# Kernel optimization log

Measured on AMD Instinct MI355X. Metric: run time of the kernel, lower is better.

Reference implementation:

```python
import jax, jax.numpy as jnp
import numpy as np

D_MODEL = 1024
N_HEADS = 16
HEAD_DIM = D_MODEL // N_HEADS


def setup_inputs() -> dict:
    key = jax.random.key(0)
    ks = jax.random.split(key, 5)
    B, T = 4, 4096
    x = jax.random.normal(ks[0], (B, T, D_MODEL), dtype=jnp.float32)
    s = 1.0 / np.sqrt(D_MODEL)
    Wqkv = jax.random.normal(ks[1], (D_MODEL, 3 * D_MODEL), dtype=jnp.float32) * s
    bqkv = jnp.zeros((3 * D_MODEL,), dtype=jnp.float32)
    Wout = jax.random.normal(ks[2], (D_MODEL, D_MODEL), dtype=jnp.float32) * s
    bout = jnp.zeros((D_MODEL,), dtype=jnp.float32)
    return {"x": x, "Wqkv": Wqkv, "bqkv": bqkv, "Wout": Wout, "bout": bout}


def _feature_map(x):
    # elu(x) + 1  (strictly positive feature map)
    return jax.nn.elu(x) + 1.0


def reference(x, Wqkv, bqkv, Wout, bout):
    B, T, C = x.shape
    H, D = N_HEADS, HEAD_DIM
    qkv = x @ Wqkv + bqkv                      # [B,T,3C]
    qkv = qkv.reshape(B, T, 3, H, D)
    qkv = jnp.transpose(qkv, (2, 0, 3, 1, 4))  # [3,B,H,T,D]
    q, k, v = qkv[0], qkv[1], qkv[2]
    scale = D ** 0.25
    q_m = _feature_map(q / scale)
    k_m = _feature_map(k / scale)
    kv = jnp.einsum('bhtd,bhtm->bhdm', k_m, v)     # [B,H,D,D]
    out = jnp.einsum('bhtd,bhdm->bhtm', q_m, kv)   # [B,H,T,D]
    z = q_m.sum(axis=-1, keepdims=True)            # note: sum over feature dim (as in source)
    out = out / (z + 1e-6)
    out = jnp.transpose(out, (0, 2, 1, 3)).reshape(B, T, C)
    return out @ Wout + bout
```

## Files before the change

### kernel.cpp

```cpp
#include <hip/hip_runtime.h>
#include <hip/hip_bf16.h>
#include <math.h>

#define B_ 4
#define T_ 4096
#define H_ 16
#define D_ 64
#define C_ 1024
#define BT_ (B_*T_)

using short8  = __attribute__((ext_vector_type(8))) short;
using floatx4 = __attribute__((ext_vector_type(4))) float;

__device__ __forceinline__ float feature_map(float x) {
    return x > 0.0f ? x + 1.0f : __expf(x);
}
__device__ __forceinline__ unsigned short f2bf(float x) {
    union { __hip_bfloat16 b; unsigned short u; } c;
    c.b = __float2bfloat16(x);
    return c.u;
}
__device__ __forceinline__ void async16(const void* g, void* l) {
    __builtin_amdgcn_global_load_lds(
        (const __attribute__((address_space(1))) void*)g,
        (__attribute__((address_space(3))) void*)l, 16, 0, 0);
}
__device__ __forceinline__ const char* sel3(const char* a0, const char* a1,
                                            const char* a2, int t) {
    return t == 0 ? a0 : (t == 1 ? a1 : a2);
}

__global__ __launch_bounds__(256)
void convert_x_kernel(const float4* __restrict__ x, ushort* __restrict__ xb)
{
    const size_t n = (size_t)BT_ * C_ / 8;
    for (size_t i = (size_t)blockIdx.x * 256 + threadIdx.x; i < n;
         i += (size_t)2048 * 256) {
        const float4 a = x[2 * i], b = x[2 * i + 1];
        short8 r;
        r[0] = (short)f2bf(a.x); r[1] = (short)f2bf(a.y);
        r[2] = (short)f2bf(a.z); r[3] = (short)f2bf(a.w);
        r[4] = (short)f2bf(b.x); r[5] = (short)f2bf(b.y);
        r[6] = (short)f2bf(b.z); r[7] = (short)f2bf(b.w);
        *reinterpret_cast<short8*>(&xb[i * 8]) = r;
    }
}

__global__ __launch_bounds__(256)
void transpose_w_kernel(const float* __restrict__ Wqkv, ushort* __restrict__ WqkvT,
                        const float* __restrict__ Wout, ushort* __restrict__ WoutT)
{
    __shared__ float t[32][33];
    const bool qkv = blockIdx.x < 96;
    const float* W  = qkv ? Wqkv : Wout;
    ushort* WT      = qkv ? WqkvT : WoutT;
    const int N     = qkv ? 3 * C_ : C_;
    const int n0 = (qkv ? blockIdx.x : blockIdx.x - 96) * 32, k0 = blockIdx.y * 32;
    const int r = threadIdx.x >> 5, c = threadIdx.x & 31;
    #pragma unroll
    for (int i = 0; i < 4; i++)
        t[r + 8 * i][c] = W[(size_t)(k0 + r + 8 * i) * N + n0 + c];
    __syncthreads();
    #pragma unroll
    for (int i = 0; i < 4; i++)
        WT[(size_t)(n0 + r + 8 * i) * C_ + k0 + c] = f2bf(t[c][r + 8 * i]);
}

#define BAR()    __builtin_amdgcn_s_barrier()
#define WAITDS() do { asm volatile("s_waitcnt lgkmcnt(0)" ::: "memory"); \
                      __builtin_amdgcn_sched_barrier(0); } while(0)
#define VM6()    do { asm volatile("s_waitcnt vmcnt(6)" ::: "memory"); \
                      __builtin_amdgcn_sched_barrier(0); } while(0)

#define LDA(slot, mf, ks, buf) \
    aR[slot][ks] = *(const short8*)(smem + (buf)*32768 + ((mf)>>2)*16384 + \
                                    aRowB + ((mf)&3)*2048 + cks##ks)
#define LDB(nf, ks, buf) \
    bR[nf][ks] = *(const short8*)(smem + 65536 + (buf)*32768 + ((nf)>>1)*16384 + \
                                  bRowB + ((nf)&1)*2048 + cks##ks)
#define LDA8(MB, BUF) do { \
    LDA(0, MB+0, 0, BUF); LDA(0, MB+0, 1, BUF); \
    LDA(1, MB+1, 0, BUF); LDA(1, MB+1, 1, BUF); \
    LDA(2, MB+2, 0, BUF); LDA(2, MB+2, 1, BUF); \
    LDA(3, MB+3, 0, BUF); LDA(3, MB+3, 1, BUF); } while(0)
#define LDB4(NF, BUF) do { \
    LDB(NF+0, 0, BUF); LDB(NF+0, 1, BUF); \
    LDB(NF+1, 0, BUF); LDB(NF+1, 1, BUF); } while(0)

#define MM(mf, nf, ks, slot) \
    acc[mf][nf] = __builtin_amdgcn_mfma_f32_16x16x32_bf16( \
        aR[slot][ks], bR[nf][ks], acc[mf][nf], 0, 0, 0)
#define MFMAQ(MB, NF) do { \
    MM(MB+0,NF+0,0,0); MM(MB+1,NF+0,0,1); MM(MB+2,NF+0,0,2); MM(MB+3,NF+0,0,3); \
    MM(MB+0,NF+1,0,0); MM(MB+1,NF+1,0,1); MM(MB+2,NF+1,0,2); MM(MB+3,NF+1,0,3); \
    MM(MB+0,NF+0,1,0); MM(MB+1,NF+0,1,1); MM(MB+2,NF+0,1,2); MM(MB+3,NF+0,1,3); \
    MM(MB+0,NF+1,1,0); MM(MB+1,NF+1,1,1); MM(MB+2,NF+1,1,2); MM(MB+3,NF+1,1,3); \
} while(0)

#define STGA(h, G, buf) do { int _g = (G); if (_g >= NTILE*16) _g -= NTILE*16; \
    const char* _b = sel3(Ab0, Ab1, Ab2, _g >> 4); const int _w = (_g & 15) * 128; \
    async16(_b + aOf##h##0 + _w, smem + (buf)*32768 + (h)*16384 + wv*1024); \
    async16(_b + aOf##h##1 + _w, smem + (buf)*32768 + (h)*16384 + 8192 + wv*1024); \
} while(0)
#define STGB(h, G, buf) do { int _g = (G); if (_g >= NTILE*16) _g -= NTILE*16; \
    const char* _b = sel3(Bb0, Bb1, Bb2, _g >> 4); const int _w = (_g & 15) * 128; \
    async16(_b + bOf##h##0 + _w, smem + 65536 + (buf)*32768 + (h)*16384 + wv*1024); \
    async16(_b + bOf##h##1 + _w, smem + 65536 + (buf)*32768 + (h)*16384 + 8192 + wv*1024); \
} while(0)

#define ITERBODY(GB) \
    const int g1 = (GB) + 2*it + 1, g2 = (GB) + 2*it + 2, g3 = (GB) + 2*it + 3; \
     BAR(); LDA8(0, 0); LDB4(0, 0); STGA(1, g1, 1); \
    WAITDS(); __builtin_amdgcn_s_setprio(1); MFMAQ(0, 0); \
    __builtin_amdgcn_s_setprio(0); \
     BAR(); LDB4(2, 0); STGA(0, g2, 0); \
    WAITDS(); __builtin_amdgcn_s_setprio(1); MFMAQ(0, 2); \
    __builtin_amdgcn_s_setprio(0); \
     BAR(); LDA8(4, 0); STGB(0, g2, 0); \
    WAITDS(); __builtin_amdgcn_s_setprio(1); MFMAQ(4, 2); \
    __builtin_amdgcn_s_setprio(0); \
     BAR(); STGB(1, g2, 0); \
    WAITDS(); __builtin_amdgcn_s_setprio(1); MFMAQ(4, 0); \
    __builtin_amdgcn_s_setprio(0); VM6(); \
     BAR(); LDA8(0, 1); LDB4(0, 1); STGA(1, g2, 0); \
    WAITDS(); __builtin_amdgcn_s_setprio(1); MFMAQ(0, 0); \
    __builtin_amdgcn_s_setprio(0); \
     BAR(); LDB4(2, 1); STGA(0, g3, 1); \
    WAITDS(); __builtin_amdgcn_s_setprio(1); MFMAQ(0, 2); \
    __builtin_amdgcn_s_setprio(0); \
     BAR(); LDA8(4, 1); STGB(0, g3, 1); \
    WAITDS(); __builtin_amdgcn_s_setprio(1); MFMAQ(4, 2); \
    __builtin_amdgcn_s_setprio(0); \
     BAR(); STGB(1, g3, 1); \
    WAITDS(); __builtin_amdgcn_s_setprio(1); MFMAQ(4, 0); \
    __builtin_amdgcn_s_setprio(0); VM6();

template<int EPI>
__device__ __forceinline__ void gemm_epilogue(
    floatx4 (&acc)[8][4], const float (&bv)[4],
    int mBase, int nBase, int wm, int wn, int lr, int quad,
    ushort* __restrict__ q_out, ushort* __restrict__ kT_out,
    ushort* __restrict__ vT_out, float* __restrict__ f_out)
{
    if (EPI == 0) {
        const float inv_scale = 0.35355339059327373f;
        const int seg = nBase >> 10;
        if (seg == 0) {
            #pragma unroll
            for (int mf = 0; mf < 8; mf++)
                #pragma unroll
                for (int i = 0; i < 4; i++) {
                    float f0 = feature_map((acc[mf][0][i] + bv[0]) * inv_scale);
                    float f1 = feature_map((acc[mf][1][i] + bv[1]) * inv_scale);
                    float f2 = feature_map((acc[mf][2][i] + bv[2]) * inv_scale);
                    float f3 = feature_map((acc[mf][3][i] + bv[3]) * inv_scale);
                    float z = f0 + f1 + f2 + f3;
                    z += __shfl_xor(z, 1); z += __shfl_xor(z, 2);
                    z += __shfl_xor(z, 4); z += __shfl_xor(z, 8);
                    const float inv = 1.0f / (z + 1e-6f);
                    const int t = mBase + wm * 128 + mf * 16 + quad * 4 + i;
                    const int cbase = nBase + wn * 64 + lr;
                    q_out[(size_t)t * C_ + cbase]      = f2bf(f0 * inv);
                    q_out[(size_t)t * C_ + cbase + 16] = f2bf(f1 * inv);
                    q_out[(size_t)t * C_ + cbase + 32] = f2bf(f2 * inv);
                    q_out[(size_t)t * C_ + cbase + 48] = f2bf(f3 * inv);
                }
        } else {
            ushort* dstT = (seg == 1) ? kT_out : vT_out;
            #pragma unroll
            for (int nf = 0; nf < 4; nf++) {
                const int c = (nBase + wn * 64 + nf * 16 + lr) & 1023;
                #pragma unroll
                for (int mf = 0; mf < 8; mf++) {
                    float v0 = acc[mf][nf][0] + bv[nf], v1 = acc[mf][nf][1] + bv[nf];
                    float v2 = acc[mf][nf][2] + bv[nf], v3 = acc[mf][nf][3] + bv[nf];
                    if (seg == 1) {
                        v0 = feature_map(v0 * inv_scale); v1 = feature_map(v1 * inv_scale);
                        v2 = feature_map(v2 * inv_scale); v3 = feature_map(v3 * inv_scale);
                    }
                    const int tt = mBase + wm * 128 + mf * 16 + quad * 4;
                    *(ushort4*)&dstT[(size_t)c * BT_ + tt] =
                        make_ushort4(f2bf(v0), f2bf(v1), f2bf(v2), f2bf(v3));
                }
            }
        }
    } else {
        #pragma unroll
        for (int nf = 0; nf < 4; nf++) {
            const int c = nBase + wn * 64 + nf * 16 + lr;
            #pragma unroll
            for (int mf = 0; mf < 8; mf++)
                #pragma unroll
                for (int i = 0; i < 4; i++) {
                    const int row = mBase + wm * 128 + mf * 16 + quad * 4 + i;
                    f_out[(size_t)row * C_ + c] = acc[mf][nf][i] + bv[nf];
                }
        }
    }
    #pragma unroll
    for (int i = 0; i < 8; i++)
        #pragma unroll
        for (int j = 0; j < 4; j++) acc[i][j] = (floatx4)0.0f;
}

template<int EPI, int NBX, int NTILE>
__device__ __forceinline__ void gemm_body(
    const ushort* __restrict__ A, const ushort* __restrict__ Bm,
    const float* __restrict__ bias,
    ushort* __restrict__ q_out, ushort* __restrict__ kT_out,
    ushort* __restrict__ vT_out, float* __restrict__ f_out)
{
    __shared__ __align__(16) unsigned char smem[131072];

    const int tid = threadIdx.x;
    const int wv = tid >> 6, l = tid & 63;
    const int wm = wv >> 2, wn = wv & 3;
    const int lr = l & 15, quad = l >> 4;

    int mB0, mB1, mB2, nB0, nB1, nB2;
    {
        const int tot = (int)gridDim.x * NTILE, cpx = tot >> 3;
        int lg0 = blockIdx.x;
        int w0 = (lg0 & 7) * cpx + (lg0 >> 3);
        mB0 = (w0 / NBX) * 256; nB0 = (w0 % NBX) * 256;
        if (NTILE > 1) {
            int lg1 = blockIdx.x + (int)gridDim.x;
            int w1 = (lg1 & 7) * cpx + (lg1 >> 3);
            mB1 = (w1 / NBX) * 256; nB1 = (w1 % NBX) * 256;
            int lg2 = blockIdx.x + 2 * (int)gridDim.x;
            int w2 = (lg2 & 7) * cpx + (lg2 >> 3);
            mB2 = (w2 / NBX) * 256; nB2 = (w2 % NBX) * 256;
        } else { mB1 = mB0; nB1 = nB0; mB2 = mB0; nB2 = nB0; }
    }
    const size_t bOffB = (EPI == 1) ? (size_t)(mB0 >> 12) * ((size_t)C_ * C_) : 0;
    const char* Ab0 = (const char*)(A + (size_t)mB0 * C_);
    const char* Ab1 = (const char*)(A + (size_t)mB1 * C_);
    const char* Ab2 = (const char*)(A + (size_t)mB2 * C_);
    const char* Bb0 = (const char*)(Bm + bOffB + (size_t)nB0 * C_);
    const char* Bb1 = (const char*)(Bm + bOffB + (size_t)nB1 * C_);
    const char* Bb2 = (const char*)(Bm + bOffB + (size_t)nB2 * C_);

    float bv0[4], bv1[4], bv2[4];
    #pragma unroll
    for (int nf = 0; nf < 4; nf++) {
        bv0[nf] = bias[nB0 + wn * 64 + nf * 16 + lr];
        bv1[nf] = (NTILE > 1) ? bias[nB1 + wn * 64 + nf * 16 + lr] : bv0[nf];
        bv2[nf] = (NTILE > 1) ? bias[nB2 + wn * 64 + nf * 16 + lr] : bv0[nf];
    }

    const int s0 = tid >> 3;
    const int cb = ((tid & 7) * 16) ^ ((s0 & 7) << 4);
    const int aOf00 = (s0)       * 2048 + cb;
    const int aOf01 = (128 + s0) * 2048 + cb;
    const int aOf10 = (64 + s0)  * 2048 + cb;
    const int aOf11 = (192 + s0) * 2048 + cb;
    const int bq    = (s0 >> 5) * 64 + (s0 & 31);
    const int bOf00 = (bq)       * 2048 + cb;
    const int bOf01 = (bq + 128) * 2048 + cb;
    const int bOf10 = (bq + 32)  * 2048 + cb;
    const int bOf11 = (bq + 160) * 2048 + cb;

    const int aRowB = (wm * 64 + lr) * 128;
    const int bRowB = (wn * 32 + lr) * 128;
    const int cks0 = (quad * 16) ^ ((lr & 7) << 4);
    const int cks1 = 64 ^ cks0;

    floatx4 acc[8][4];
    #pragma unroll
    for (int i = 0; i < 8; i++)
        #pragma unroll
        for (int j = 0; j < 4; j++) acc[i][j] = (floatx4)0.0f;
    short8 aR[4][2], bR[4][2];

    STGA(0, 0, 0); STGB(0, 0, 0); STGB(1, 0, 0); STGA(1, 0, 0);
    STGA(0, 1, 1); STGB(0, 1, 1); STGB(1, 1, 1);
    asm volatile("s_waitcnt vmcnt(6)" ::: "memory");
    __builtin_amdgcn_sched_barrier(0);

    #pragma unroll 1
    for (int it = 0; it < 8; ++it) { ITERBODY(0) }
    gemm_epilogue<EPI>(acc, bv0, mB0, nB0, wm, wn, lr, quad,
                       q_out, kT_out, vT_out, f_out);
    if (NTILE > 1) {
        #pragma unroll 1
        for (int it = 0; it < 8; ++it) { ITERBODY(16) }
        gemm_epilogue<EPI>(acc, bv1, mB1, nB1, wm, wn, lr, quad,
                           q_out, kT_out, vT_out, f_out);
        #pragma unroll 1
        for (int it = 0; it < 8; ++it) { ITERBODY(32) }
        gemm_epilogue<EPI>(acc, bv2, mB2, nB2, wm, wn, lr, quad,
                           q_out, kT_out, vT_out, f_out);
    }
    asm volatile("s_waitcnt vmcnt(0)" ::: "memory");
}

__global__ __launch_bounds__(512, 2)
void qkv8_kernel(const ushort* __restrict__ A, const ushort* __restrict__ Bm,
                 const float* __restrict__ bias, ushort* __restrict__ q_out,
                 ushort* __restrict__ kT_out, ushort* __restrict__ vT_out)
{
    gemm_body<0, 12, 3>(A, Bm, bias, q_out, kT_out, vT_out, nullptr);
}

__global__ __launch_bounds__(512, 2)
void outproj8_kernel(const ushort* __restrict__ A, const ushort* __restrict__ Bm,
                     const float* __restrict__ bias, float* __restrict__ f_out)
{
    gemm_body<1, 4, 1>(A, Bm, bias, nullptr, nullptr, nullptr, f_out);
}

__global__ __launch_bounds__(256)
void kv_accum_kernel(const ushort* __restrict__ kmT, const ushort* __restrict__ vT,
                     float* __restrict__ kv)
{
    const int tid = threadIdx.x;
    const int w = tid >> 6, l = tid & 63;
    const int wm = w >> 1, wn = w & 1;
    const int lr = l & 15, quad = l >> 4;
    const int bh = blockIdx.y;
    const int b = bh >> 4, h = bh & 15;
    const size_t t0 = (size_t)b * T_ + (size_t)blockIdx.x * 256;

    const ushort* Ar = kmT + (size_t)(h * 64 + wm * 32 + lr) * BT_ + t0 + quad * 8;
    const ushort* Br = vT  + (size_t)(h * 64 + wn * 32 + lr) * BT_ + t0 + quad * 8;

    floatx4 acc[2][2];
    #pragma unroll
    for (int i = 0; i < 2; i++)
        #pragma unroll
        for (int j = 0; j < 2; j++) acc[i][j] = (floatx4)0.0f;

    #pragma unroll
    for (int tt = 0; tt < 256; tt += 32) {
        const short8 af0 = *(const short8*)&Ar[tt];
        const short8 af1 = *(const short8*)&Ar[(size_t)16 * BT_ + tt];
        const short8 bf0 = *(const short8*)&Br[tt];
        const short8 bf1 = *(const short8*)&Br[(size_t)16 * BT_ + tt];
        acc[0][0] = __builtin_amdgcn_mfma_f32_16x16x32_bf16(af0, bf0, acc[0][0], 0, 0, 0);
        acc[0][1] = __builtin_amdgcn_mfma_f32_16x16x32_bf16(af0, bf1, acc[0][1], 0, 0, 0);
        acc[1][0] = __builtin_amdgcn_mfma_f32_16x16x32_bf16(af1, bf0, acc[1][0], 0, 0, 0);
        acc[1][1] = __builtin_amdgcn_mfma_f32_16x16x32_bf16(af1, bf1, acc[1][1], 0, 0, 0);
    }

    float* kvb = kv + (size_t)bh * (D_ * D_);
    #pragma unroll
    for (int i = 0; i < 2; i++)
        #pragma unroll
        for (int j = 0; j < 2; j++)
            #pragma unroll
            for (int r = 0; r < 4; r++) {
                const int d = wm * 32 + i * 16 + quad * 4 + r;
                const int m = wn * 32 + j * 16 + lr;
                atomicAdd(&kvb[d * 64 + m], acc[i][j][r]);
            }
}

__global__ __launch_bounds__(256)
void kw_kernel(const float* __restrict__ kv, const ushort* __restrict__ WoutT,
               ushort* __restrict__ KWT)
{
    const int tid = threadIdx.x;
    const int w = tid >> 6, l = tid & 63;
    const int lr = l & 15, quad = l >> 4;
    const int bh = blockIdx.y, b = bh >> 4, h = bh & 15;
    const int c0 = blockIdx.x * 256 + w * 64;

    const float* kvb = kv + (size_t)bh * (D_ * D_);

    short8 bf[4][2];
    #pragma unroll
    for (int df = 0; df < 4; df++)
        #pragma unroll
        for (int ks = 0; ks < 2; ks++) {
            const float* src = &kvb[(df * 16 + lr) * 64 + ks * 32 + quad * 8];
            const float4 u0 = *(const float4*)src;
            const float4 u1 = *(const float4*)(src + 4);
            short8 t;
            t[0] = (short)f2bf(u0.x); t[1] = (short)f2bf(u0.y);
            t[2] = (short)f2bf(u0.z); t[3] = (short)f2bf(u0.w);
            t[4] = (short)f2bf(u1.x); t[5] = (short)f2bf(u1.y);
            t[6] = (short)f2bf(u1.z); t[7] = (short)f2bf(u1.w);
            bf[df][ks] = t;
        }

    floatx4 acc[4][4];
    #pragma unroll
    for (int i = 0; i < 4; i++)
        #pragma unroll
        for (int j = 0; j < 4; j++) acc[i][j] = (floatx4)0.0f;

    #pragma unroll
    for (int ks = 0; ks < 2; ks++) {
        short8 af[4];
        #pragma unroll
        for (int cf = 0; cf < 4; cf++)
            af[cf] = *(const short8*)&WoutT[(size_t)(c0 + cf * 16 + lr) * C_
                                            + h * 64 + ks * 32 + quad * 8];
        #pragma unroll
        for (int cf = 0; cf < 4; cf++)
            #pragma unroll
            for (int df = 0; df < 4; df++)
                acc[cf][df] = __builtin_amdgcn_mfma_f32_16x16x32_bf16(
                    af[cf], bf[df][ks], acc[cf][df], 0, 0, 0);
    }

    ushort* dst = KWT + (size_t)b * (C_ * C_);
    #pragma unroll
    for (int cf = 0; cf < 4; cf++)
        #pragma unroll
        for (int i = 0; i < 4; i++) {
            const int c = c0 + cf * 16 + quad * 4 + i;
            #pragma unroll
            for (int df = 0; df < 4; df++)
                dst[(size_t)c * C_ + h * 64 + df * 16 + lr] = f2bf(acc[cf][df][i]);
        }
}

extern "C" void kernel_launch(void* const* d_in, const int* in_sizes, int n_in,
                              void* d_out, int out_size, void* d_ws, size_t ws_size,
                              hipStream_t stream)
{
    const float* x    = (const float*)d_in[0];
    const float* Wqkv = (const float*)d_in[1];
    const float* bqkv = (const float*)d_in[2];
    const float* Wout = (const float*)d_in[3];
    const float* bout = (const float*)d_in[4];
    float* out = (float*)d_out;

    char* ws = (char*)d_ws;
    ushort* xb     = (ushort*)ws;
    ushort* WqkvT  = (ushort*)(ws + 33554432);
    ushort* WoutT  = (ushort*)(ws + 39845888);
    ushort* qs     = (ushort*)(ws + 41943040);
    float*  kv     = (float*) (ws + 75497472);
    ushort* KWT    = (ushort*)ws;
    ushort* kmT    = (ushort*)d_out;
    ushort* vT     = (ushort*)((char*)d_out + 33554432);

    hipMemsetAsync(kv, 0, (size_t)B_ * H_ * D_ * D_ * sizeof(float), stream);

    convert_x_kernel<<<2048, 256, 0, stream>>>((const float4*)x, xb);
    transpose_w_kernel<<<dim3(128, 32), 256, 0, stream>>>(Wqkv, WqkvT, Wout, WoutT);

    qkv8_kernel<<<dim3(256), 512, 0, stream>>>(xb, WqkvT, bqkv, qs, kmT, vT);
    kv_accum_kernel<<<dim3(16, B_ * H_), 256, 0, stream>>>(kmT, vT, kv);
    kw_kernel<<<dim3(4, B_ * H_), 256, 0, stream>>>(kv, WoutT, KWT);
    outproj8_kernel<<<dim3(256), 512, 0, stream>>>(qs, KWT, bout, out);
}
```

Before: 311.8 us.

## Merge prep kernels and replace kv atomics with split partial sums

Merges the x-conversion and weight-transpose kernels into a single launch that dispatches on block index. It also replaces the atomicAdd accumulation of kv (and the memset that zeroed it) with 8 per-split partial buffers that kv_accum writes plainly. kw_kernel then sums those partials while loading. This removes one kernel launch, a memset, and atomic contention, in exchange for extra partial-buffer traffic and 8x reads in kw_kernel.

```diff
diff --git a/kernel.cpp b/kernel.cpp
--- a/kernel.cpp
+++ b/kernel.cpp
@@ -31,39 +31,41 @@
 }
 
 __global__ __launch_bounds__(256)
-void convert_x_kernel(const float4* __restrict__ x, ushort* __restrict__ xb)
-{
-    const size_t n = (size_t)BT_ * C_ / 8;
-    for (size_t i = (size_t)blockIdx.x * 256 + threadIdx.x; i < n;
-         i += (size_t)2048 * 256) {
-        const float4 a = x[2 * i], b = x[2 * i + 1];
-        short8 r;
-        r[0] = (short)f2bf(a.x); r[1] = (short)f2bf(a.y);
-        r[2] = (short)f2bf(a.z); r[3] = (short)f2bf(a.w);
-        r[4] = (short)f2bf(b.x); r[5] = (short)f2bf(b.y);
-        r[6] = (short)f2bf(b.z); r[7] = (short)f2bf(b.w);
-        *reinterpret_cast<short8*>(&xb[i * 8]) = r;
-    }
-}
-
-__global__ __launch_bounds__(256)
-void transpose_w_kernel(const float* __restrict__ Wqkv, ushort* __restrict__ WqkvT,
-                        const float* __restrict__ Wout, ushort* __restrict__ WoutT)
+void prep_kernel(const float4* __restrict__ x, ushort* __restrict__ xb,
+                 const float* __restrict__ Wqkv, ushort* __restrict__ WqkvT,
+                 const float* __restrict__ Wout, ushort* __restrict__ WoutT)
 {
     __shared__ float t[32][33];
-    const bool qkv = blockIdx.x < 96;
-    const float* W  = qkv ? Wqkv : Wout;
-    ushort* WT      = qkv ? WqkvT : WoutT;
-    const int N     = qkv ? 3 * C_ : C_;
-    const int n0 = (qkv ? blockIdx.x : blockIdx.x - 96) * 32, k0 = blockIdx.y * 32;
-    const int r = threadIdx.x >> 5, c = threadIdx.x & 31;
-    #pragma unroll
-    for (int i = 0; i < 4; i++)
-        t[r + 8 * i][c] = W[(size_t)(k0 + r + 8 * i) * N + n0 + c];
-    __syncthreads();
-    #pragma unroll
-    for (int i = 0; i < 4; i++)
-        WT[(size_t)(n0 + r + 8 * i) * C_ + k0 + c] = f2bf(t[c][r + 8 * i]);
+    const int bx = blockIdx.x;
+    if (bx < 2048) {
+        const size_t n = (size_t)BT_ * C_ / 8;
+        for (size_t i = (size_t)bx * 256 + threadIdx.x; i < n;
+             i += (size_t)2048 * 256) {
+            const float4 a = x[2 * i], b = x[2 * i + 1];
+            short8 r;
+            r[0] = (short)f2bf(a.x); r[1] = (short)f2bf(a.y);
+            r[2] = (short)f2bf(a.z); r[3] = (short)f2bf(a.w);
+            r[4] = (short)f2bf(b.x); r[5] = (short)f2bf(b.y);
+            r[6] = (short)f2bf(b.z); r[7] = (short)f2bf(b.w);
+            *reinterpret_cast<short8*>(&xb[i * 8]) = r;
+        }
+    } else {
+        const int id = bx - 2048;
+        const int xi = id & 127, y = id >> 7;
+        const bool qkv = xi < 96;
+        const float* W  = qkv ? Wqkv : Wout;
+        ushort* WT      = qkv ? WqkvT : WoutT;
+        const int N     = qkv ? 3 * C_ : C_;
+        const int n0 = (qkv ? xi : xi - 96) * 32, k0 = y * 32;
+        const int r = threadIdx.x >> 5, c = threadIdx.x & 31;
+        #pragma unroll
+        for (int i = 0; i < 4; i++)
+            t[r + 8 * i][c] = W[(size_t)(k0 + r + 8 * i) * N + n0 + c];
+        __syncthreads();
+        #pragma unroll
+        for (int i = 0; i < 4; i++)
+            WT[(size_t)(n0 + r + 8 * i) * C_ + k0 + c] = f2bf(t[c][r + 8 * i]);
+    }
 }
 
 #define BAR()    __builtin_amdgcn_s_barrier()
@@ -311,7 +313,7 @@
 
 __global__ __launch_bounds__(256)
 void kv_accum_kernel(const ushort* __restrict__ kmT, const ushort* __restrict__ vT,
-                     float* __restrict__ kv)
+                     float* __restrict__ kv_part)
 {
     const int tid = threadIdx.x;
     const int w = tid >> 6, l = tid & 63;
@@ -319,7 +321,7 @@
     const int lr = l & 15, quad = l >> 4;
     const int bh = blockIdx.y;
     const int b = bh >> 4, h = bh & 15;
-    const size_t t0 = (size_t)b * T_ + (size_t)blockIdx.x * 256;
+    const size_t t0 = (size_t)b * T_ + (size_t)blockIdx.x * 512;
 
     const ushort* Ar = kmT + (size_t)(h * 64 + wm * 32 + lr) * BT_ + t0 + quad * 8;
     const ushort* Br = vT  + (size_t)(h * 64 + wn * 32 + lr) * BT_ + t0 + quad * 8;
@@ -330,8 +332,8 @@
         #pragma unroll
         for (int j = 0; j < 2; j++) acc[i][j] = (floatx4)0.0f;
 
-    #pragma unroll
-    for (int tt = 0; tt < 256; tt += 32) {
+    #pragma unroll 8
+    for (int tt = 0; tt < 512; tt += 32) {
         const short8 af0 = *(const short8*)&Ar[tt];
         const short8 af1 = *(const short8*)&Ar[(size_t)16 * BT_ + tt];
         const short8 bf0 = *(const short8*)&Br[tt];
@@ -342,7 +344,7 @@
         acc[1][1] = __builtin_amdgcn_mfma_f32_16x16x32_bf16(af1, bf1, acc[1][1], 0, 0, 0);
     }
 
-    float* kvb = kv + (size_t)bh * (D_ * D_);
+    float* kvb = kv_part + ((size_t)blockIdx.x * 64 + bh) * (D_ * D_);
     #pragma unroll
     for (int i = 0; i < 2; i++)
         #pragma unroll
@@ -351,12 +353,12 @@
             for (int r = 0; r < 4; r++) {
                 const int d = wm * 32 + i * 16 + quad * 4 + r;
                 const int m = wn * 32 + j * 16 + lr;
-                atomicAdd(&kvb[d * 64 + m], acc[i][j][r]);
+                kvb[d * 64 + m] = acc[i][j][r];
             }
 }
 
 __global__ __launch_bounds__(256)
-void kw_kernel(const float* __restrict__ kv, const ushort* __restrict__ WoutT,
+void kw_kernel(const float* __restrict__ kv_part, const ushort* __restrict__ WoutT,
                ushort* __restrict__ KWT)
 {
     const int tid = threadIdx.x;
@@ -365,16 +367,22 @@
     const int bh = blockIdx.y, b = bh >> 4, h = bh & 15;
     const int c0 = blockIdx.x * 256 + w * 64;
 
-    const float* kvb = kv + (size_t)bh * (D_ * D_);
-
     short8 bf[4][2];
     #pragma unroll
     for (int df = 0; df < 4; df++)
         #pragma unroll
         for (int ks = 0; ks < 2; ks++) {
-            const float* src = &kvb[(df * 16 + lr) * 64 + ks * 32 + quad * 8];
-            const float4 u0 = *(const float4*)src;
-            const float4 u1 = *(const float4*)(src + 4);
+            const int off = (df * 16 + lr) * 64 + ks * 32 + quad * 8;
+            float4 u0 = make_float4(0.f, 0.f, 0.f, 0.f);
+            float4 u1 = make_float4(0.f, 0.f, 0.f, 0.f);
+            #pragma unroll
+            for (int s = 0; s < 8; s++) {
+                const float* src = kv_part + ((size_t)s * 64 + bh) * (D_ * D_) + off;
+                const float4 a0 = *(const float4*)src;
+                const float4 a1 = *(const float4*)(src + 4);
+                u0.x += a0.x; u0.y += a0.y; u0.z += a0.z; u0.w += a0.w;
+                u1.x += a1.x; u1.y += a1.y; u1.z += a1.z; u1.w += a1.w;
+            }
             short8 t;
             t[0] = (short)f2bf(u0.x); t[1] = (short)f2bf(u0.y);
             t[2] = (short)f2bf(u0.z); t[3] = (short)f2bf(u0.w);
@@ -428,22 +436,20 @@
     float* out = (float*)d_out;
 
     char* ws = (char*)d_ws;
-    ushort* xb     = (ushort*)ws;
-    ushort* WqkvT  = (ushort*)(ws + 33554432);
-    ushort* WoutT  = (ushort*)(ws + 39845888);
-    ushort* qs     = (ushort*)(ws + 41943040);
-    float*  kv     = (float*) (ws + 75497472);
-    ushort* KWT    = (ushort*)ws;
-    ushort* kmT    = (ushort*)d_out;
-    ushort* vT     = (ushort*)((char*)d_out + 33554432);
-
-    hipMemsetAsync(kv, 0, (size_t)B_ * H_ * D_ * D_ * sizeof(float), stream);
-
-    convert_x_kernel<<<2048, 256, 0, stream>>>((const float4*)x, xb);
-    transpose_w_kernel<<<dim3(128, 32), 256, 0, stream>>>(Wqkv, WqkvT, Wout, WoutT);
+    ushort* xb      = (ushort*)ws;
+    ushort* WqkvT   = (ushort*)(ws + 33554432);
+    ushort* WoutT   = (ushort*)(ws + 39845888);
+    ushort* qs      = (ushort*)(ws + 41943040);
+    ushort* KWT     = (ushort*)ws;
+    float*  kv_part = (float*)(ws + 8388608);
+    ushort* kmT     = (ushort*)d_out;
+    ushort* vT      = (ushort*)((char*)d_out + 33554432);
+
+    prep_kernel<<<6144, 256, 0, stream>>>((const float4*)x, xb,
+                                          Wqkv, WqkvT, Wout, WoutT);
 
     qkv8_kernel<<<dim3(256), 512, 0, stream>>>(xb, WqkvT, bqkv, qs, kmT, vT);
-    kv_accum_kernel<<<dim3(16, B_ * H_), 256, 0, stream>>>(kmT, vT, kv);
-    kw_kernel<<<dim3(4, B_ * H_), 256, 0, stream>>>(kv, WoutT, KWT);
+    kv_accum_kernel<<<dim3(8, B_ * H_), 256, 0, stream>>>(kmT, vT, kv_part);
+    kw_kernel<<<dim3(4, B_ * H_), 256, 0, stream>>>(kv_part, WoutT, KWT);
     outproj8_kernel<<<dim3(256), 512, 0, stream>>>(qs, KWT, bout, out);
 }
```

After: 309.6 us. Within noise of the previous version (-0.7%).
